# Optimization experiments

Hardware: AMD Instinct MI355X
Metric: run time of the kernel (lower is better)

The kernel has to match this reference:

```python
import jax, jax.numpy as jnp
import numpy as np

# Irreps per layer: 128x0e + 64x1o + 32x2e  (same for all K layers)
M0, M1, M2 = 128, 64, 32          # multiplicities of l=0,1,2
D_S, D_V, HID = 256, 64, 64       # output scalar dim, vector channels, score MLP hidden
K, N = 4, 80000
D_IN = M0 + 3 * M1 + 5 * M2       # 480
D_SC = D_S + 2 * D_V              # 384 = score-MLP input dim (D_s + dim_v_out//3)
EPS = 1e-5


def setup_inputs() -> dict:
    key = jax.random.key(0)
    ks = jax.random.split(key, 20)
    f32 = jnp.float32
    d = {}
    for k in range(K):
        d[f"x{k}"] = jax.random.normal(ks[k], (N, D_IN), f32)
    # e3nn o3.Linear weights: N(0,1), normalized by 1/sqrt(fan_in) at apply time
    d["W_l0"] = jax.random.normal(ks[4], (K, M0, M0), f32)
    d["W_l1"] = jax.random.normal(ks[5], (K, M1, M1), f32)
    d["W_l2"] = jax.random.normal(ks[6], (K, M2, M2), f32)
    # FullyConnectedTensorProduct weights (1o x 1o -> 0e and 1o x 1o -> 1e)
    d["W_tp0"] = jax.random.normal(ks[7], (M1, M1), f32)
    d["W_tp1"] = jax.random.normal(ks[8], (M1, M1), f32)
    d_in_s = M0 + M2 + 1  # s_k (+) Frobenius norms (+) p0
    d["Ws"] = jax.random.normal(ks[9], (K, d_in_s, D_S), f32) / np.sqrt(d_in_s)
    d["bs"] = jnp.zeros((K, D_S), f32)
    # vector_proj: o3.Linear(64x1o + 1x1e -> 64x1o + 64x1e); 1o->1o and 1e->1e paths
    d["Wv1o"] = jax.random.normal(ks[10], (K, M1, D_V), f32)
    d["Wv1e"] = jax.random.normal(ks[11], (K, D_V), f32)
    d["gamma"] = jnp.ones((D_SC,), f32)
    d["beta"] = jnp.zeros((D_SC,), f32)
    d["Wm1"] = jax.random.normal(ks[12], (D_SC, HID), f32) / np.sqrt(D_SC)
    d["bm1"] = jnp.zeros((HID,), f32)
    d["Wm2"] = jax.random.normal(ks[13], (HID, 1), f32) / np.sqrt(HID)
    d["bm2"] = jnp.zeros((1,), f32)
    return d


def _forward(x0, x1, x2, x3, W_l0, W_l1, W_l2, W_tp0, W_tp1, Ws, bs,
             Wv1o, Wv1e, gamma, beta, Wm1, bm1, Wm2, bm2):
    xs = [x0, x1, x2, x3]
    n = x0.shape[0]
    inv0, inv1, inv2 = 1.0 / np.sqrt(M0), 1.0 / np.sqrt(M1), 1.0 / np.sqrt(M2)
    s_list, v_list = [], []
    v_prev = None
    for k in range(K):
        x = xs[k]
        x_s = x[:, :M0]                                   # [N, 128] l=0
        x_v = x[:, M0:M0 + 3 * M1].reshape(n, M1, 3)      # [N, 64, 3] l=1
        x_T = x[:, M0 + 3 * M1:].reshape(n, M2, 5)        # [N, 32, 5] l=2
        # Step 4.1: equivariant projections (o3.Linear mixes channels per m)
        s_k = (x_s @ W_l0[k]) * inv0                       # [N, 128]
        v_k = jnp.einsum('nim,ij->njm', x_v, W_l1[k]) * inv1  # [N, 64, 3]
        T_k = jnp.einsum('nim,ij->njm', x_T, W_l2[k]) * inv2  # [N, 32, 5]
        n_k = jnp.linalg.norm(T_k, axis=-1)                # [N, 32] Frobenius norms
        # Step 4.2: cross-layer CG tensor products (k=0 boundary -> zeros)
        if k > 0:
            u0 = jnp.einsum('nim,ij->njm', v_k, W_tp0)
            p0 = (u0 * v_prev).sum(axis=(1, 2))[:, None] / (np.sqrt(3.0) * M1)  # [N,1]
            u1 = jnp.einsum('nim,ij->njm', v_k, W_tp1)
            p1 = jnp.cross(u1, v_prev).sum(axis=1) / (np.sqrt(2.0) * M1)        # [N,3]
        else:
            p0 = jnp.zeros((n, 1), x.dtype)
            p1 = jnp.zeros((n, 3), x.dtype)
        v_prev = v_k
        # Step 4.4a: unified projections
        s_tilde = jnp.concatenate([s_k, n_k, p0], axis=-1) @ Ws[k] + bs[k]      # [N, 256]
        v1o = jnp.einsum('nim,ij->njm', v_k, Wv1o[k]) * inv1                    # [N, 64, 3]
        v1e = p1[:, None, :] * Wv1e[k][None, :, None]                           # [N, 64, 3]
        v_tilde = jnp.concatenate([v1o.reshape(n, -1), v1e.reshape(n, -1)], axis=-1)  # [N, 384]
        s_list.append(s_tilde)
        v_list.append(v_tilde)
    S = jnp.stack(s_list, axis=1)   # [N, K, D_S]
    V = jnp.stack(v_list, axis=1)   # [N, K, 6*D_V]
    # Step 4.3: JK attention over layers
    m = jnp.linalg.norm(V.reshape(n, K, 2 * D_V, 3), axis=-1)   # [N, K, 128]
    score_in = jnp.concatenate([S, m], axis=-1)                 # [N, K, 384]
    mu = score_in.mean(axis=-1, keepdims=True)
    var = score_in.var(axis=-1, keepdims=True)
    h = (score_in - mu) / jnp.sqrt(var + EPS) * gamma + beta
    e = jax.nn.silu(h @ Wm1 + bm1) @ Wm2 + bm2                  # [N, K, 1]
    alpha = jax.nn.softmax(e, axis=1)
    # Step 4.4b: weighted collapse over K
    return ((alpha * S).sum(axis=1), (alpha * V).sum(axis=1))


def reference(x0, x1, x2, x3, W_l0, W_l1, W_l2, W_tp0, W_tp1, Ws, bs,
              Wv1o, Wv1e, gamma, beta, Wm1, bm1, Wm2, bm2):
    return _forward(x0, x1, x2, x3, W_l0, W_l1, W_l2, W_tp0, W_tp1, Ws, bs,
                    Wv1o, Wv1e, gamma, beta, Wm1, bm1, Wm2, bm2)
```

## Files before the change

kernel.cpp:

```cpp
#include <hip/hip_runtime.h>
#include <math.h>

#define NTHR 64
#define ROWS 4
#define N_ROWS 80000
#define PU 488
#define PC 164
#define PV 196

__device__ __forceinline__ float wsum64(float v) {
  #pragma unroll
  for (int m = 1; m < 64; m <<= 1) v += __shfl_xor(v, m, 64);
  return v;
}

__device__ __forceinline__ void contract64(const float* __restrict__ W, int j0,
                                           const float* lds, int pitch, int off,
                                           float acc[3][ROWS]) {
  #pragma unroll 2
  for (int ic = 0; ic < 16; ++ic) {
    float wt[4];
    #pragma unroll
    for (int ii = 0; ii < 4; ++ii) wt[ii] = W[(ic * 4 + ii) * 64 + j0];
    #pragma unroll
    for (int r = 0; r < ROWS; ++r) {
      const float* p = lds + r * pitch + off + ic * 12;
      float4 q0 = *(const float4*)p;
      float4 q1 = *(const float4*)(p + 4);
      float4 q2 = *(const float4*)(p + 8);
      float xv[12] = {q0.x,q0.y,q0.z,q0.w, q1.x,q1.y,q1.z,q1.w, q2.x,q2.y,q2.z,q2.w};
      #pragma unroll
      for (int ii = 0; ii < 4; ++ii)
        #pragma unroll
        for (int m = 0; m < 3; ++m)
          acc[m][r] = fmaf(xv[ii * 3 + m], wt[ii], acc[m][r]);
    }
  }
}

__global__ __launch_bounds__(NTHR, 4)
void efb_kernel(const float* __restrict__ x0, const float* __restrict__ x1,
                const float* __restrict__ x2, const float* __restrict__ x3,
                const float* __restrict__ Wl0, const float* __restrict__ Wl1,
                const float* __restrict__ Wl2, const float* __restrict__ Wtp0,
                const float* __restrict__ Wtp1, const float* __restrict__ Wsm,
                const float* __restrict__ bsv, const float* __restrict__ Wv1o,
                const float* __restrict__ Wv1e, const float* __restrict__ gma,
                const float* __restrict__ bta, const float* __restrict__ Wm1,
                const float* __restrict__ bm1, const float* __restrict__ Wm2,
                const float* __restrict__ bm2, float* __restrict__ out)
{
  __shared__ float U[ROWS * PU];
  __shared__ float cat[ROWS * PC];
  __shared__ float vbuf[ROWS * PV];

  const int lane = threadIdx.x;
  const int j0 = lane;
  const int j2 = lane & 31, half = lane >> 5;
  const int row0 = blockIdx.x * ROWS;

  const float INV0 = 0.08838834764831845f;
  const float INV1 = 0.125f;
  const float INV2 = 0.17677669529663687f;
  const float P0S  = 0.009021097956087907f;
  const float P1S  = 0.011048543456039806f;

  float Nm0[4][ROWS];
  float vnum[3][ROWS];
  float ne[3][ROWS];
  float vpr[3][ROWS];
  float mx[ROWS], Zz[ROWS];
  #pragma unroll
  for (int r = 0; r < ROWS; ++r) {
    mx[r] = -1e30f; Zz[r] = 0.f;
    #pragma unroll
    for (int t = 0; t < 4; ++t) Nm0[t][r] = 0.f;
    #pragma unroll
    for (int m = 0; m < 3; ++m) { vnum[m][r] = 0.f; ne[m][r] = 0.f; vpr[m][r] = 0.f; }
  }

  for (int k = 0; k < 4; ++k) {
    const float* gx = (k == 0) ? x0 : (k == 1) ? x1 : (k == 2) ? x2 : x3;
    gx += (size_t)row0 * 480;

    __syncthreads();
    #pragma unroll
    for (int r = 0; r < ROWS; ++r)
      for (int c = lane; c < 120; c += 64) {
        float4 q = ((const float4*)gx)[r * 120 + c];
        *(float4*)&U[r * PU + c * 4] = q;
      }
    __syncthreads();

    {
      const float* W = Wl0 + k * 16384;
      float a0[ROWS] = {}, a1[ROWS] = {};
      #pragma unroll 2
      for (int ic = 0; ic < 32; ++ic) {
        float wt0[4], wt1[4];
        #pragma unroll
        for (int ii = 0; ii < 4; ++ii) {
          wt0[ii] = W[(ic * 4 + ii) * 128 + j0];
          wt1[ii] = W[(ic * 4 + ii) * 128 + 64 + j0];
        }
        #pragma unroll
        for (int r = 0; r < ROWS; ++r) {
          float4 q = *(const float4*)&U[r * PU + ic * 4];
          float xv[4] = {q.x, q.y, q.z, q.w};
          #pragma unroll
          for (int ii = 0; ii < 4; ++ii) {
            a0[r] = fmaf(xv[ii], wt0[ii], a0[r]);
            a1[r] = fmaf(xv[ii], wt1[ii], a1[r]);
          }
        }
      }
      #pragma unroll
      for (int r = 0; r < ROWS; ++r) {
        cat[r * PC + j0]      = a0[r] * INV0;
        cat[r * PC + 64 + j0] = a1[r] * INV0;
      }
    }

    float vtmp[3][ROWS];
    {
      float ac[3][ROWS] = {};
      contract64(Wl1 + k * 4096, j0, U, PU, 128, ac);
      #pragma unroll
      for (int r = 0; r < ROWS; ++r)
        #pragma unroll
        for (int m = 0; m < 3; ++m) {
          vtmp[m][r] = ac[m][r] * INV1;
          vbuf[r * PV + j0 * 3 + m] = vtmp[m][r];
        }
    }

    {
      constexpr int RH = ROWS / 2;
      const float* W = Wl2 + k * 1024;
      float t5[5][RH] = {};
      #pragma unroll 2
      for (int ic = 0; ic < 8; ++ic) {
        float wt[4];
        #pragma unroll
        for (int ii = 0; ii < 4; ++ii) wt[ii] = W[(ic * 4 + ii) * 32 + j2];
        #pragma unroll
        for (int rr = 0; rr < RH; ++rr) {
          const float* p = &U[(half * RH + rr) * PU + 320 + ic * 20];
          float xt[20];
          #pragma unroll
          for (int q4 = 0; q4 < 5; ++q4) {
            float4 q = *(const float4*)(p + q4 * 4);
            xt[q4*4] = q.x; xt[q4*4+1] = q.y; xt[q4*4+2] = q.z; xt[q4*4+3] = q.w;
          }
          #pragma unroll
          for (int ii = 0; ii < 4; ++ii)
            #pragma unroll
            for (int m = 0; m < 5; ++m)
              t5[m][rr] = fmaf(xt[ii * 5 + m], wt[ii], t5[m][rr]);
        }
      }
      #pragma unroll
      for (int rr = 0; rr < RH; ++rr) {
        float s = 0.f;
        #pragma unroll
        for (int m = 0; m < 5; ++m) { float tt = t5[m][rr] * INV2; s = fmaf(tt, tt, s); }
        cat[(half * RH + rr) * PC + 128 + j2] = sqrtf(s);
      }
    }
    __syncthreads();

    float p1[3][ROWS], np1[ROWS];
    if (k > 0) {
      {
        float u0[3][ROWS] = {};
        contract64(Wtp0, j0, vbuf, PV, 0, u0);
        #pragma unroll
        for (int r = 0; r < ROWS; ++r) {
          float s = 0.f;
          #pragma unroll
          for (int m = 0; m < 3; ++m) s = fmaf(u0[m][r], vpr[m][r], s);
          s = wsum64(s) * P0S;
          if (lane == r) cat[r * PC + 160] = s;
        }
      }
      {
        float u1[3][ROWS] = {};
        contract64(Wtp1, j0, vbuf, PV, 0, u1);
        #pragma unroll
        for (int r = 0; r < ROWS; ++r) {
          float c0 = u1[1][r] * vpr[2][r] - u1[2][r] * vpr[1][r];
          float c1 = u1[2][r] * vpr[0][r] - u1[0][r] * vpr[2][r];
          float c2 = u1[0][r] * vpr[1][r] - u1[1][r] * vpr[0][r];
          p1[0][r] = wsum64(c0) * P1S;
          p1[1][r] = wsum64(c1) * P1S;
          p1[2][r] = wsum64(c2) * P1S;
          np1[r] = sqrtf(p1[0][r]*p1[0][r] + p1[1][r]*p1[1][r] + p1[2][r]*p1[2][r]);
        }
      }
    } else {
      #pragma unroll
      for (int r = 0; r < ROWS; ++r) {
        #pragma unroll
        for (int m = 0; m < 3; ++m) p1[m][r] = 0.f;
        np1[r] = 0.f;
        if (lane == r) cat[r * PC + 160] = 0.f;
      }
    }
    #pragma unroll
    for (int r = 0; r < ROWS; ++r)
      #pragma unroll
      for (int m = 0; m < 3; ++m) vpr[m][r] = vtmp[m][r];
    __syncthreads();

    {
      const float* W = Wsm + k * 41216;
      float ac4[4][ROWS] = {};
      #pragma unroll 2
      for (int ic = 0; ic < 40; ++ic) {
        float w4[4][4];
        #pragma unroll
        for (int ii = 0; ii < 4; ++ii)
          #pragma unroll
          for (int t = 0; t < 4; ++t) w4[ii][t] = W[(ic * 4 + ii) * 256 + t * 64 + j0];
        #pragma unroll
        for (int r = 0; r < ROWS; ++r) {
          float4 q = *(const float4*)&cat[r * PC + ic * 4];
          float cv[4] = {q.x, q.y, q.z, q.w};
          #pragma unroll
          for (int ii = 0; ii < 4; ++ii)
            #pragma unroll
            for (int t = 0; t < 4; ++t)
              ac4[t][r] = fmaf(cv[ii], w4[ii][t], ac4[t][r]);
        }
      }
      {
        float w4[4];
        #pragma unroll
        for (int t = 0; t < 4; ++t) w4[t] = W[160 * 256 + t * 64 + j0];
        #pragma unroll
        for (int r = 0; r < ROWS; ++r) {
          float c = cat[r * PC + 160];
          #pragma unroll
          for (int t = 0; t < 4; ++t) ac4[t][r] = fmaf(c, w4[t], ac4[t][r]);
        }
      }
      float bt[4];
      #pragma unroll
      for (int t = 0; t < 4; ++t) bt[t] = bsv[k * 256 + t * 64 + j0];
      #pragma unroll
      for (int r = 0; r < ROWS; ++r)
        #pragma unroll
        for (int t = 0; t < 4; ++t)
          U[r * PU + t * 64 + j0] = ac4[t][r] + bt[t];
    }

    float vo[3][ROWS], mbS[ROWS], mbE[ROWS];
    float wv = Wv1e[k * 64 + j0];
    {
      float ac[3][ROWS] = {};
      contract64(Wv1o + k * 4096, j0, vbuf, PV, 0, ac);
      float awv = fabsf(wv);
      #pragma unroll
      for (int r = 0; r < ROWS; ++r) {
        float s = 0.f;
        #pragma unroll
        for (int m = 0; m < 3; ++m) { vo[m][r] = ac[m][r] * INV1; s = fmaf(vo[m][r], vo[m][r], s); }
        mbS[r] = sqrtf(s);
        mbE[r] = np1[r] * awv;
        U[r * PU + 260 + j0] = mbS[r];
        U[r * PU + 260 + 64 + j0] = mbE[r];
      }
    }
    __syncthreads();

    float mu8[ROWS], rs8[ROWS];
    #pragma unroll
    for (int r = 0; r < ROWS; ++r) {
      float s = 0.f, sq = 0.f;
      #pragma unroll
      for (int t = 0; t < 4; ++t) {
        float v = U[r * PU + t * 64 + j0];
        s += v; sq = fmaf(v, v, sq);
      }
      s += mbS[r] + mbE[r];
      sq = fmaf(mbS[r], mbS[r], sq); sq = fmaf(mbE[r], mbE[r], sq);
      s = wsum64(s); sq = wsum64(sq);
      mu8[r] = s * (1.f / 384.f);
      float var = sq * (1.f / 384.f) - mu8[r] * mu8[r];
      rs8[r] = rsqrtf(var + 1e-5f);
    }

    float E8[ROWS];
    {
      float A8[ROWS] = {};
      float B0 = 0.f, C0 = 0.f;
      #pragma unroll 2
      for (int ic = 0; ic < 64; ++ic) {
        float wv4[4], gv4[4], bv4[4];
        #pragma unroll
        for (int ii = 0; ii < 4; ++ii) {
          int f = ic * 4 + ii;
          wv4[ii] = Wm1[f * 64 + j0]; gv4[ii] = gma[f]; bv4[ii] = bta[f];
        }
        float gw[4];
        #pragma unroll
        for (int ii = 0; ii < 4; ++ii) {
          gw[ii] = gv4[ii] * wv4[ii];
          B0 += gw[ii];
          C0 = fmaf(bv4[ii], wv4[ii], C0);
        }
        #pragma unroll
        for (int r = 0; r < ROWS; ++r) {
          float4 q = *(const float4*)&U[r * PU + ic * 4];
          float xv[4] = {q.x, q.y, q.z, q.w};
          #pragma unroll
          for (int ii = 0; ii < 4; ++ii) A8[r] = fmaf(xv[ii], gw[ii], A8[r]);
        }
      }
      #pragma unroll 2
      for (int ic = 0; ic < 32; ++ic) {
        float wv4[4], gv4[4], bv4[4];
        #pragma unroll
        for (int ii = 0; ii < 4; ++ii) {
          int f = 256 + ic * 4 + ii;
          wv4[ii] = Wm1[f * 64 + j0]; gv4[ii] = gma[f]; bv4[ii] = bta[f];
        }
        float gw[4];
        #pragma unroll
        for (int ii = 0; ii < 4; ++ii) {
          gw[ii] = gv4[ii] * wv4[ii];
          B0 += gw[ii];
          C0 = fmaf(bv4[ii], wv4[ii], C0);
        }
        #pragma unroll
        for (int r = 0; r < ROWS; ++r) {
          float4 q = *(const float4*)&U[r * PU + 260 + ic * 4];
          float xv[4] = {q.x, q.y, q.z, q.w};
          #pragma unroll
          for (int ii = 0; ii < 4; ++ii) A8[r] = fmaf(xv[ii], gw[ii], A8[r]);
        }
      }
      float b1 = bm1[j0], w2 = Wm2[j0], b2v = bm2[0];
      #pragma unroll
      for (int r = 0; r < ROWS; ++r) {
        float y = rs8[r] * (A8[r] - mu8[r] * B0) + C0 + b1;
        float sl = y / (1.f + expf(-y));
        E8[r] = wsum64(sl * w2) + b2v;
      }
    }

    #pragma unroll
    for (int r = 0; r < ROWS; ++r) {
      float mxn = fmaxf(mx[r], E8[r]);
      float rf = expf(mx[r] - mxn);
      float w = expf(E8[r] - mxn);
      Zz[r] = Zz[r] * rf + w;
      mx[r] = mxn;
      #pragma unroll
      for (int t = 0; t < 4; ++t) {
        float skv = U[r * PU + t * 64 + j0];
        Nm0[t][r] = fmaf(Nm0[t][r], rf, w * skv);
      }
      #pragma unroll
      for (int m = 0; m < 3; ++m) {
        vnum[m][r] = fmaf(vnum[m][r], rf, w * vo[m][r]);
        ne[m][r]   = fmaf(ne[m][r],   rf, w * (p1[m][r] * wv));
      }
    }
  }

  __syncthreads();
  float iz[ROWS];
  #pragma unroll
  for (int r = 0; r < ROWS; ++r) iz[r] = 1.f / Zz[r];
  #pragma unroll
  for (int r = 0; r < ROWS; ++r)
    #pragma unroll
    for (int t = 0; t < 4; ++t)
      out[(size_t)(row0 + r) * 256 + t * 64 + j0] = Nm0[t][r] * iz[r];
  #pragma unroll
  for (int r = 0; r < ROWS; ++r)
    #pragma unroll
    for (int m = 0; m < 3; ++m) {
      U[r * PU + j0 * 3 + m]       = vnum[m][r] * iz[r];
      U[r * PU + 192 + j0 * 3 + m] = ne[m][r] * iz[r];
    }
  __syncthreads();
  const size_t o1 = (size_t)N_ROWS * 256;
  #pragma unroll
  for (int r = 0; r < ROWS; ++r)
    for (int c = lane; c < 96; c += 64) {
      float4 q = *(const float4*)&U[r * PU + c * 4];
      *(float4*)&out[o1 + (size_t)(row0 + r) * 384 + c * 4] = q;
    }
}

extern "C" void kernel_launch(void* const* d_in, const int* in_sizes, int n_in,
                              void* d_out, int out_size, void* d_ws, size_t ws_size,
                              hipStream_t stream) {
  const float* x0   = (const float*)d_in[0];
  const float* x1   = (const float*)d_in[1];
  const float* x2   = (const float*)d_in[2];
  const float* x3   = (const float*)d_in[3];
  const float* Wl0  = (const float*)d_in[4];
  const float* Wl1  = (const float*)d_in[5];
  const float* Wl2  = (const float*)d_in[6];
  const float* Wtp0 = (const float*)d_in[7];
  const float* Wtp1 = (const float*)d_in[8];
  const float* Wsm  = (const float*)d_in[9];
  const float* bsv  = (const float*)d_in[10];
  const float* Wv1o = (const float*)d_in[11];
  const float* Wv1e = (const float*)d_in[12];
  const float* gma  = (const float*)d_in[13];
  const float* bta  = (const float*)d_in[14];
  const float* Wm1  = (const float*)d_in[15];
  const float* bm1  = (const float*)d_in[16];
  const float* Wm2  = (const float*)d_in[17];
  const float* bm2  = (const float*)d_in[18];
  float* out = (float*)d_out;

  dim3 grid(N_ROWS / ROWS), block(NTHR);
  efb_kernel<<<grid, block, 0, stream>>>(
      x0, x1, x2, x3, Wl0, Wl1, Wl2, Wtp0, Wtp1, Wsm, bsv,
      Wv1o, Wv1e, gma, bta, Wm1, bm1, Wm2, bm2, out);
}
```

Baseline: 4.764 ms.

## Pack four independent wavefronts per block and keep scalar outputs in registers

```diff
diff --git a/kernel.cpp b/kernel.cpp
--- a/kernel.cpp
+++ b/kernel.cpp
@@ -1,8 +1,10 @@
 #include <hip/hip_runtime.h>
 #include <math.h>
 
-#define NTHR 64
+#define NTHR 256
+#define WPB 4
 #define ROWS 4
+#define RPB (WPB * ROWS)
 #define N_ROWS 80000
 #define PU 488
 #define PC 164
@@ -38,7 +40,7 @@
   }
 }
 
-__global__ __launch_bounds__(NTHR, 4)
+__global__ __launch_bounds__(NTHR, 3)
 void efb_kernel(const float* __restrict__ x0, const float* __restrict__ x1,
                 const float* __restrict__ x2, const float* __restrict__ x3,
                 const float* __restrict__ Wl0, const float* __restrict__ Wl1,
@@ -50,14 +52,20 @@
                 const float* __restrict__ bm1, const float* __restrict__ Wm2,
                 const float* __restrict__ bm2, float* __restrict__ out)
 {
-  __shared__ float U[ROWS * PU];
-  __shared__ float cat[ROWS * PC];
-  __shared__ float vbuf[ROWS * PV];
-
-  const int lane = threadIdx.x;
+  __shared__ float U[WPB * ROWS * PU];
+  __shared__ float cat[WPB * ROWS * PC];
+  __shared__ float vbuf[WPB * ROWS * PV];
+
+  const int tid = threadIdx.x;
+  const int wid = tid >> 6;
+  const int lane = tid & 63;
   const int j0 = lane;
   const int j2 = lane & 31, half = lane >> 5;
-  const int row0 = blockIdx.x * ROWS;
+
+  float* Uw  = U    + wid * ROWS * PU;
+  float* catw = cat + wid * ROWS * PC;
+  float* vbw = vbuf + wid * ROWS * PV;
+  const int row0 = blockIdx.x * RPB + wid * ROWS;
 
   const float INV0 = 0.08838834764831845f;
   const float INV1 = 0.125f;
@@ -88,7 +96,7 @@
     for (int r = 0; r < ROWS; ++r)
       for (int c = lane; c < 120; c += 64) {
         float4 q = ((const float4*)gx)[r * 120 + c];
-        *(float4*)&U[r * PU + c * 4] = q;
+        *(float4*)&Uw[r * PU + c * 4] = q;
       }
     __syncthreads();
 
@@ -105,7 +113,7 @@
         }
         #pragma unroll
         for (int r = 0; r < ROWS; ++r) {
-          float4 q = *(const float4*)&U[r * PU + ic * 4];
+          float4 q = *(const float4*)&Uw[r * PU + ic * 4];
           float xv[4] = {q.x, q.y, q.z, q.w};
           #pragma unroll
           for (int ii = 0; ii < 4; ++ii) {
@@ -116,21 +124,21 @@
       }
       #pragma unroll
       for (int r = 0; r < ROWS; ++r) {
-        cat[r * PC + j0]      = a0[r] * INV0;
-        cat[r * PC + 64 + j0] = a1[r] * INV0;
+        catw[r * PC + j0]      = a0[r] * INV0;
+        catw[r * PC + 64 + j0] = a1[r] * INV0;
       }
     }
 
     float vtmp[3][ROWS];
     {
       float ac[3][ROWS] = {};
-      contract64(Wl1 + k * 4096, j0, U, PU, 128, ac);
+      contract64(Wl1 + k * 4096, j0, Uw, PU, 128, ac);
       #pragma unroll
       for (int r = 0; r < ROWS; ++r)
         #pragma unroll
         for (int m = 0; m < 3; ++m) {
           vtmp[m][r] = ac[m][r] * INV1;
-          vbuf[r * PV + j0 * 3 + m] = vtmp[m][r];
+          vbw[r * PV + j0 * 3 + m] = vtmp[m][r];
         }
     }
 
@@ -145,7 +153,7 @@
         for (int ii = 0; ii < 4; ++ii) wt[ii] = W[(ic * 4 + ii) * 32 + j2];
         #pragma unroll
         for (int rr = 0; rr < RH; ++rr) {
-          const float* p = &U[(half * RH + rr) * PU + 320 + ic * 20];
+          const float* p = &Uw[(half * RH + rr) * PU + 320 + ic * 20];
           float xt[20];
           #pragma unroll
           for (int q4 = 0; q4 < 5; ++q4) {
@@ -164,7 +172,7 @@
         float s = 0.f;
         #pragma unroll
         for (int m = 0; m < 5; ++m) { float tt = t5[m][rr] * INV2; s = fmaf(tt, tt, s); }
-        cat[(half * RH + rr) * PC + 128 + j2] = sqrtf(s);
+        catw[(half * RH + rr) * PC + 128 + j2] = sqrtf(s);
       }
     }
     __syncthreads();
@@ -173,19 +181,19 @@
     if (k > 0) {
       {
         float u0[3][ROWS] = {};
-        contract64(Wtp0, j0, vbuf, PV, 0, u0);
+        contract64(Wtp0, j0, vbw, PV, 0, u0);
         #pragma unroll
         for (int r = 0; r < ROWS; ++r) {
           float s = 0.f;
           #pragma unroll
           for (int m = 0; m < 3; ++m) s = fmaf(u0[m][r], vpr[m][r], s);
           s = wsum64(s) * P0S;
-          if (lane == r) cat[r * PC + 160] = s;
+          if (lane == r) catw[r * PC + 160] = s;
         }
       }
       {
         float u1[3][ROWS] = {};
-        contract64(Wtp1, j0, vbuf, PV, 0, u1);
+        contract64(Wtp1, j0, vbw, PV, 0, u1);
         #pragma unroll
         for (int r = 0; r < ROWS; ++r) {
           float c0 = u1[1][r] * vpr[2][r] - u1[2][r] * vpr[1][r];
@@ -203,7 +211,7 @@
         #pragma unroll
         for (int m = 0; m < 3; ++m) p1[m][r] = 0.f;
         np1[r] = 0.f;
-        if (lane == r) cat[r * PC + 160] = 0.f;
+        if (lane == r) catw[r * PC + 160] = 0.f;
       }
     }
     #pragma unroll
@@ -212,6 +220,7 @@
       for (int m = 0; m < 3; ++m) vpr[m][r] = vtmp[m][r];
     __syncthreads();
 
+    float sk[4][ROWS];
     {
       const float* W = Wsm + k * 41216;
       float ac4[4][ROWS] = {};
@@ -224,7 +233,7 @@
           for (int t = 0; t < 4; ++t) w4[ii][t] = W[(ic * 4 + ii) * 256 + t * 64 + j0];
         #pragma unroll
         for (int r = 0; r < ROWS; ++r) {
-          float4 q = *(const float4*)&cat[r * PC + ic * 4];
+          float4 q = *(const float4*)&catw[r * PC + ic * 4];
           float cv[4] = {q.x, q.y, q.z, q.w};
           #pragma unroll
           for (int ii = 0; ii < 4; ++ii)
@@ -239,7 +248,7 @@
         for (int t = 0; t < 4; ++t) w4[t] = W[160 * 256 + t * 64 + j0];
         #pragma unroll
         for (int r = 0; r < ROWS; ++r) {
-          float c = cat[r * PC + 160];
+          float c = catw[r * PC + 160];
           #pragma unroll
           for (int t = 0; t < 4; ++t) ac4[t][r] = fmaf(c, w4[t], ac4[t][r]);
         }
@@ -250,15 +259,17 @@
       #pragma unroll
       for (int r = 0; r < ROWS; ++r)
         #pragma unroll
-        for (int t = 0; t < 4; ++t)
-          U[r * PU + t * 64 + j0] = ac4[t][r] + bt[t];
+        for (int t = 0; t < 4; ++t) {
+          sk[t][r] = ac4[t][r] + bt[t];
+          Uw[r * PU + t * 64 + j0] = sk[t][r];
+        }
     }
 
     float vo[3][ROWS], mbS[ROWS], mbE[ROWS];
     float wv = Wv1e[k * 64 + j0];
     {
       float ac[3][ROWS] = {};
-      contract64(Wv1o + k * 4096, j0, vbuf, PV, 0, ac);
+      contract64(Wv1o + k * 4096, j0, vbw, PV, 0, ac);
       float awv = fabsf(wv);
       #pragma unroll
       for (int r = 0; r < ROWS; ++r) {
@@ -267,8 +278,8 @@
         for (int m = 0; m < 3; ++m) { vo[m][r] = ac[m][r] * INV1; s = fmaf(vo[m][r], vo[m][r], s); }
         mbS[r] = sqrtf(s);
         mbE[r] = np1[r] * awv;
-        U[r * PU + 260 + j0] = mbS[r];
-        U[r * PU + 260 + 64 + j0] = mbE[r];
+        Uw[r * PU + 260 + j0] = mbS[r];
+        Uw[r * PU + 260 + 64 + j0] = mbE[r];
       }
     }
     __syncthreads();
@@ -279,7 +290,7 @@
       float s = 0.f, sq = 0.f;
       #pragma unroll
       for (int t = 0; t < 4; ++t) {
-        float v = U[r * PU + t * 64 + j0];
+        float v = sk[t][r];
         s += v; sq = fmaf(v, v, sq);
       }
       s += mbS[r] + mbE[r];
@@ -311,7 +322,7 @@
         }
         #pragma unroll
         for (int r = 0; r < ROWS; ++r) {
-          float4 q = *(const float4*)&U[r * PU + ic * 4];
+          float4 q = *(const float4*)&Uw[r * PU + ic * 4];
           float xv[4] = {q.x, q.y, q.z, q.w};
           #pragma unroll
           for (int ii = 0; ii < 4; ++ii) A8[r] = fmaf(xv[ii], gw[ii], A8[r]);
@@ -334,7 +345,7 @@
         }
         #pragma unroll
         for (int r = 0; r < ROWS; ++r) {
-          float4 q = *(const float4*)&U[r * PU + 260 + ic * 4];
+          float4 q = *(const float4*)&Uw[r * PU + 260 + ic * 4];
           float xv[4] = {q.x, q.y, q.z, q.w};
           #pragma unroll
           for (int ii = 0; ii < 4; ++ii) A8[r] = fmaf(xv[ii], gw[ii], A8[r]);
@@ -357,10 +368,8 @@
       Zz[r] = Zz[r] * rf + w;
       mx[r] = mxn;
       #pragma unroll
-      for (int t = 0; t < 4; ++t) {
-        float skv = U[r * PU + t * 64 + j0];
-        Nm0[t][r] = fmaf(Nm0[t][r], rf, w * skv);
-      }
+      for (int t = 0; t < 4; ++t)
+        Nm0[t][r] = fmaf(Nm0[t][r], rf, w * sk[t][r]);
       #pragma unroll
       for (int m = 0; m < 3; ++m) {
         vnum[m][r] = fmaf(vnum[m][r], rf, w * vo[m][r]);
@@ -382,15 +391,15 @@
   for (int r = 0; r < ROWS; ++r)
     #pragma unroll
     for (int m = 0; m < 3; ++m) {
-      U[r * PU + j0 * 3 + m]       = vnum[m][r] * iz[r];
-      U[r * PU + 192 + j0 * 3 + m] = ne[m][r] * iz[r];
+      Uw[r * PU + j0 * 3 + m]       = vnum[m][r] * iz[r];
+      Uw[r * PU + 192 + j0 * 3 + m] = ne[m][r] * iz[r];
     }
   __syncthreads();
   const size_t o1 = (size_t)N_ROWS * 256;
   #pragma unroll
   for (int r = 0; r < ROWS; ++r)
     for (int c = lane; c < 96; c += 64) {
-      float4 q = *(const float4*)&U[r * PU + c * 4];
+      float4 q = *(const float4*)&Uw[r * PU + c * 4];
       *(float4*)&out[o1 + (size_t)(row0 + r) * 384 + c * 4] = q;
     }
 }
@@ -419,7 +428,7 @@
   const float* bm2  = (const float*)d_in[18];
   float* out = (float*)d_out;
 
-  dim3 grid(N_ROWS / ROWS), block(NTHR);
+  dim3 grid(N_ROWS / RPB), block(NTHR);
   efb_kernel<<<grid, block, 0, stream>>>(
       x0, x1, x2, x3, Wl0, Wl1, Wl2, Wtp0, Wtp1, Wsm, bsv,
       Wv1o, Wv1e, gma, bta, Wm1, bm1, Wm2, bm2, out);
```

After: 4.078 ms. 14.4% less time.
